# Kernel tuning notes

Hardware: AMD Instinct MI355X
Metric: run time of the kernel (lower is better)

## Reference

```python
import jax, jax.numpy as jnp
import numpy as np

B, L, D, H, K = 4, 2048, 256, 8, 32
DH = D // H
DE = 64          # d_edge
CLIP = 32        # relpos_clip


def _ln(x, g, b):
    mu = x.mean(-1, keepdims=True)
    var = ((x - mu) ** 2).mean(-1, keepdims=True)
    return (x - mu) / jnp.sqrt(var + 1e-5) * g + b


def _gelu(x):
    return jax.nn.gelu(x, approximate=False)  # torch nn.GELU default = exact erf


def _masked_softmax(logits, mask):
    logits = jnp.where(mask == 0, jnp.finfo(logits.dtype).min, logits)
    return jax.nn.softmax(logits, axis=-1)


def setup_inputs() -> dict:
    key = jax.random.key(0)
    ks = jax.random.split(key, 24)
    s = 0.02
    w = lambda i, shape: jax.random.normal(ks[i], shape, jnp.float32) * s
    p = {}
    p['x'] = jax.random.normal(ks[0], (B, L, D), jnp.float32)
    p['mask'] = jax.random.randint(ks[1], (B, L), 0, 2, jnp.int32)
    p['nbr_idx'] = jax.random.randint(ks[2], (B, L, K), 0, L, jnp.int32)
    p['nbr_mask'] = jax.random.randint(ks[3], (B, L, K), 0, 2, jnp.int32)
    p['rel_pos'] = jax.random.randint(ks[4], (B, L, K), 0, 2 * CLIP + 1, jnp.int32)
    p['g1'] = jnp.ones((D,)); p['b1'] = jnp.zeros((D,))
    p['wq'] = w(5, (D, D)); p['wk'] = w(6, (D, D)); p['wv'] = w(7, (D, D))
    p['relpos_emb'] = w(8, (2 * CLIP + 1, DE))
    p['we1'] = w(9, (DE, D)); p['be1'] = jnp.zeros((D,))
    p['we2'] = w(10, (D, 1)); p['be2'] = jnp.zeros((1,))
    p['wg1'] = w(11, (2 * D, D)); p['bg1'] = jnp.zeros((D,))
    p['wg2'] = w(12, (D, D)); p['bg2'] = jnp.zeros((D,))
    p['wlo'] = w(13, (D, D)); p['blo'] = jnp.zeros((D,))
    p['wqkv'] = w(14, (D, 3 * D)); p['wgo'] = w(15, (D, D))
    p['wf1'] = w(16, (D, D)); p['bf1'] = jnp.zeros((D,))
    p['wf2'] = w(17, (D, 2)); p['bf2'] = jnp.zeros((2,))
    p['g2'] = jnp.ones((D,)); p['b2'] = jnp.zeros((D,))
    p['wff1'] = w(18, (D, 4 * D)); p['bff1'] = jnp.zeros((4 * D,))
    p['wff2'] = w(19, (4 * D, D)); p['bff2'] = jnp.zeros((D,))
    return p


def _block(x, mask, nbr_idx, nbr_mask, rel_pos,
           g1, b1, wq, wk, wv, relpos_emb, we1, be1, we2, be2,
           wg1, bg1, wg2, bg2, wlo, blo, wqkv, wgo,
           wf1, bf1, wf2, bf2, g2, b2, wff1, bff1, wff2, bff2):
    mf = mask.astype(x.dtype)                       # [B,L]
    h = _ln(x, g1, b1)

    # ---- local graph attention (gather over K neighbors) ----
    neigh = jax.vmap(lambda hb, ib: hb[ib])(h, nbr_idx)     # [B,L,K,D]
    q = (h @ wq)[:, :, None, :]                             # [B,L,1,D]
    k = neigh @ wk                                          # [B,L,K,D]
    v = neigh @ wv
    attn = (q * k).sum(-1) / np.sqrt(D).astype(np.float32)  # [B,L,K]
    rel = jnp.clip(rel_pos, -CLIP, CLIP) + CLIP
    e = relpos_emb[rel]                                     # [B,L,K,DE]
    attn = attn + (_gelu(e @ we1 + be1) @ we2 + be2)[..., 0]
    amask = nbr_mask * mask[:, :, None]
    w = _masked_softmax(attn, amask)
    agg = jnp.einsum('blk,blkd->bld', w, v)
    agg = agg @ wlo + blo
    g = jax.nn.sigmoid(_gelu(jnp.concatenate([h, agg], -1) @ wg1 + bg1) @ wg2 + bg2)
    h_local = (h + g * agg) * mf[..., None]

    # ---- global linear attention ----
    qkv = h @ wqkv
    qg, kg, vg = jnp.split(qkv, 3, axis=-1)
    to_heads = lambda z: z.reshape(B, L, H, DH).transpose(0, 2, 1, 3)  # [B,H,L,DH]
    qg, kg, vg = to_heads(qg), to_heads(kg), to_heads(vg)
    phi = lambda z: jax.nn.elu(z) + 1.0
    qg, kg = phi(qg), phi(kg)
    m = mf[:, None, :, None]
    kg = kg * m
    vg = vg * m
    kv = jnp.einsum('bhld,bhlm->bhdm', kg, vg)
    z = 1.0 / (jnp.einsum('bhld,bhd->bhl', qg, kg.sum(axis=2)) + 1e-6)
    y = jnp.einsum('bhld,bhdm->bhlm', qg, kv) * z[..., None]
    y = y.transpose(0, 2, 1, 3).reshape(B, L, D)
    y = (y @ wgo) * mf[..., None]
    h_global = h + y

    # ---- gated fusion (softmax over 2 branches) ----
    fw = jax.nn.softmax(_gelu(h @ wf1 + bf1) @ wf2 + bf2, axis=-1)
    yc = fw[..., 0:1] * h_local + fw[..., 1:2] * h_global
    x2 = x + (yc - x)  # DropPath is identity in eval mode

    # ---- FFN ----
    hn = _ln(x2, g2, b2)
    ffn = _gelu(hn @ wff1 + bff1) @ wff2 + bff2
    out = (x2 + ffn) * mf[..., None]
    return out


def reference(x, mask, nbr_idx, nbr_mask, rel_pos,
              g1, b1, wq, wk, wv, relpos_emb, we1, be1, we2, be2,
              wg1, bg1, wg2, bg2, wlo, blo, wqkv, wgo,
              wf1, bf1, wf2, bf2, g2, b2, wff1, bff1, wff2, bff2):
    return _block(x, mask, nbr_idx, nbr_mask, rel_pos,
                  g1, b1, wq, wk, wv, relpos_emb, we1, be1, we2, be2,
                  wg1, bg1, wg2, bg2, wlo, blo, wqkv, wgo,
                  wf1, bf1, wf2, bf2, g2, b2, wff1, bff1, wff2, bff2)
```

## Files before the change

kernel.cpp:

```cpp
#include <hip/hip_runtime.h>
#include <math.h>

#define LSEQ 2048
#define BB 4
#define DD 256
#define NROWS (BB*LSEQ)
#define LDBIG 1792

typedef unsigned short u16;
typedef unsigned int u32;
typedef short s16x8 __attribute__((ext_vector_type(8)));
typedef float f32x4 __attribute__((ext_vector_type(4)));

#define WT_BIG  0
#define WT_LO   458752
#define WT_G1   524288
#define WT_G2   655360
#define WT_GO   720896
#define WT_FF1  786432
#define WT_FF2  1048576

__device__ __forceinline__ float gelu_f(float x){
    return 0.5f*x*(1.0f+erff(x*0.70710678118654752440f));
}
__device__ __forceinline__ float phi_f(float z){ return z>0.f ? z+1.f : expf(z); }
__device__ __forceinline__ float bf2f(u16 u){ union{u32 i; float f;} x; x.i = ((u32)u)<<16; return x.f; }
__device__ __forceinline__ u16 f2bf(float f){ union{float f; u32 i;} x; x.f = f; u32 r = (x.i + 0x7fff + ((x.i>>16)&1)) >> 16; return (u16)r; }

struct TransDesc { const float* src; int dstoff; int srcK; int N; int dstStride; int tstart; };
struct TransArgs { TransDesc d[11]; };

__global__ __launch_bounds__(256) void prep_kernel(
    TransArgs args, u16* __restrict__ WT,
    const float* __restrict__ x, const float* __restrict__ g1,
    const float* __restrict__ b1, u16* __restrict__ h,
    const float* __restrict__ emb, const float* __restrict__ we1,
    const float* __restrict__ be1, const float* __restrict__ we2,
    const float* __restrict__ be2, float* __restrict__ btab,
    float* __restrict__ kvz,
    const float* __restrict__ wlo, const float* __restrict__ wg1,
    const float* __restrict__ blo, const float* __restrict__ bg1,
    float* __restrict__ bprime)
{
    int bid = blockIdx.x;
    if (bid < 1216){
        int z = 0;
        #pragma unroll
        for (int i=1;i<11;++i) if (bid >= args.d[i].tstart) z = i;
        TransDesc e = args.d[z];
        int tid = bid - e.tstart;
        int ntx = e.N >> 5;
        int kt = tid / ntx, nt = tid - kt*ntx;
        __shared__ float tile[32][33];
        int tx = threadIdx.x & 31, ty = threadIdx.x >> 5;
        #pragma unroll
        for (int i=0;i<4;++i){
            int k = kt*32 + ty + i*8;
            tile[ty+i*8][tx] = e.src[(size_t)k*e.N + nt*32 + tx];
        }
        __syncthreads();
        #pragma unroll
        for (int i=0;i<4;++i){
            int n = nt*32 + ty + i*8;
            WT[e.dstoff + (size_t)n*e.dstStride + kt*32 + tx] = f2bf(tile[tx][ty+i*8]);
        }
    } else if (bid < 9408){
        int r = bid - 1216; int t = threadIdx.x;
        size_t i = (size_t)r*DD + t;
        float v = x[i];
        float s = v, ss = v*v;
        #pragma unroll
        for (int o=32;o>=1;o>>=1){ s += __shfl_xor(s,o); ss += __shfl_xor(ss,o); }
        __shared__ float sh[8];
        int wave = t>>6, lane = t&63;
        if (lane==0){ sh[wave]=s; sh[4+wave]=ss; }
        __syncthreads();
        float S  = sh[0]+sh[1]+sh[2]+sh[3];
        float SS = sh[4]+sh[5]+sh[6]+sh[7];
        float mu  = S*(1.f/DD);
        float var = SS*(1.f/DD) - mu*mu;
        float inv = rsqrtf(var + 1e-5f);
        h[i] = f2bf((v-mu)*inv*g1[t] + b1[t]);
    } else if (bid < 9473){
        int r = bid - 9408; int j = threadIdx.x;
        float acc = be1[j];
        #pragma unroll 8
        for (int d=0; d<64; ++d) acc += emb[r*64+d]*we1[d*256+j];
        float tv = gelu_f(acc)*we2[j];
        #pragma unroll
        for (int o=32;o>=1;o>>=1) tv += __shfl_xor(tv,o);
        __shared__ float sh2[4];
        int wave = j>>6, lane = j&63;
        if (lane==0) sh2[wave]=tv;
        __syncthreads();
        if (j==0) btab[r] = sh2[0]+sh2[1]+sh2[2]+sh2[3] + be2[0];
    } else if (bid < 9605){
        int idx = (bid - 9473)*256 + threadIdx.x;
        kvz[idx] = 0.f;
    } else if (bid < 9861){
        int n = bid - 9605; int t = threadIdx.x;
        __shared__ float shc[256];
        shc[t] = wg1[(size_t)(256+t)*256 + n];
        __syncthreads();
        const float* wr = wlo + (size_t)t*256;
        float a = 0.f;
        #pragma unroll 8
        for (int m=0;m<256;++m) a += wr[m]*shc[m];
        WT[WT_G1 + (size_t)n*512 + 256 + t] = f2bf(a);
    } else {
        int t = threadIdx.x;
        float a = bg1[t];
        for (int m=0;m<256;++m) a += blo[m]*wg1[(size_t)(256+m)*256 + t];
        bprime[t] = a;
    }
}

template<int ACT, bool FINAL, typename CT>
__device__ __forceinline__ void mgemm_core(
    const u16* __restrict__ A0, const u16* __restrict__ A1, int kswitch, int lda,
    const u16* __restrict__ WT, int Kd,
    const float* __restrict__ bias, int actcol,
    CT* __restrict__ C, int ldc,
    const u16* __restrict__ addsrc, const int* __restrict__ rowmask,
    int row0, int col0)
{
    __shared__ u16 ldsA[4096];
    __shared__ u16 ldsB[8192];
    int t = threadIdx.x;
    int l = t & 63, w = t >> 6;
    int wm = w >> 1, wn = w & 1;

    int s_ar = t >> 2, s_ao = t & 3;
    int aidx1 = (s_ar>>4)*1024 + s_ao*128 + (s_ar&15)*8;
    int aidx2 = aidx1 + 4*128;
    int s_bc = t >> 1, s_bo = (t & 1)*4;
    int bbase = (s_bc>>4)*1024 + (s_bc&15)*8;

    f32x4 acc[2][4];
    #pragma unroll
    for (int mf=0;mf<2;++mf)
        #pragma unroll
        for (int nf=0;nf<4;++nf)
            acc[mf][nf] = (f32x4){0.f,0.f,0.f,0.f};

    uint4 av1, av2, bv0, bv1, bv2, bv3;
    {
        const u16* ap = A0 + (size_t)(row0+s_ar)*lda;
        av1 = *(const uint4*)(ap + s_ao*8);
        av2 = *(const uint4*)(ap + 32 + s_ao*8);
        const u16* bp = WT + (size_t)(col0 + s_bc)*Kd + s_bo*8;
        bv0 = *(const uint4*)(bp); bv1 = *(const uint4*)(bp+8);
        bv2 = *(const uint4*)(bp+16); bv3 = *(const uint4*)(bp+24);
    }

    for (int k0 = 0; k0 < Kd; k0 += 64){
        __syncthreads();
        *(uint4*)&ldsA[aidx1] = av1;
        *(uint4*)&ldsA[aidx2] = av2;
        *(uint4*)&ldsB[bbase + (s_bo  )*128] = bv0;
        *(uint4*)&ldsB[bbase + (s_bo+1)*128] = bv1;
        *(uint4*)&ldsB[bbase + (s_bo+2)*128] = bv2;
        *(uint4*)&ldsB[bbase + (s_bo+3)*128] = bv3;
        __syncthreads();
        int kn = k0 + 64;
        if (kn < Kd){
            const u16* Ab = A0; int kk = kn;
            if (kn >= kswitch){ Ab = A1; kk = kn - kswitch; }
            const u16* ap = Ab + (size_t)(row0+s_ar)*lda + kk;
            av1 = *(const uint4*)(ap + s_ao*8);
            av2 = *(const uint4*)(ap + 32 + s_ao*8);
            const u16* bp = WT + (size_t)(col0 + s_bc)*Kd + kn + s_bo*8;
            bv0 = *(const uint4*)(bp); bv1 = *(const uint4*)(bp+8);
            bv2 = *(const uint4*)(bp+16); bv3 = *(const uint4*)(bp+24);
        }
        #pragma unroll
        for (int s=0;s<2;++s){
            s16x8 af[2], bfr[4];
            #pragma unroll
            for (int mf=0;mf<2;++mf) af[mf] = *(s16x8*)&ldsA[(wm*2+mf)*1024 + (s*4+(l>>4))*128 + (l&15)*8];
            #pragma unroll
            for (int nf=0;nf<4;++nf) bfr[nf] = *(s16x8*)&ldsB[(wn*4+nf)*1024 + (s*4+(l>>4))*128 + (l&15)*8];
            #pragma unroll
            for (int mf=0; mf<2; ++mf)
                #pragma unroll
                for (int nf=0; nf<4; ++nf)
                    acc[mf][nf] = __builtin_amdgcn_mfma_f32_16x16x32_bf16(af[mf], bfr[nf], acc[mf][nf], 0,0,0);
        }
    }

    int lrow = (l>>4)*4, lcol = l&15;
    #pragma unroll
    for (int mf=0; mf<2; ++mf){
        #pragma unroll
        for (int nf=0; nf<4; ++nf){
            int col = col0 + wn*64 + nf*16 + lcol;
            float bv;
            if (ACT==1) bv = (col >= actcol) ? bias[col-actcol] : 0.f;
            else        bv = bias ? bias[col] : 0.f;
            #pragma unroll
            for (int i=0;i<4;++i){
                int row = row0 + wm*32 + mf*16 + lrow + i;
                float v = acc[mf][nf][i] + bv;
                if (ACT==1){ if (col >= actcol) v = gelu_f(v); }
                else if (ACT==2) v = 1.f/(1.f+expf(-v));
                if (FINAL){
                    float mfv = (float)rowmask[row];
                    v = (bf2f(addsrc[(size_t)row*ldc + col]) + v) * mfv;
                }
                if constexpr (sizeof(CT)==2) C[(size_t)row*ldc+col] = (CT)f2bf(v);
                else                         C[(size_t)row*ldc+col] = v;
            }
        }
    }
}

template<int ACT, bool FINAL, typename CT>
__global__ __launch_bounds__(256) void mgemm(
    const u16* __restrict__ A0, const u16* __restrict__ A1, int kswitch, int lda,
    const u16* __restrict__ WT, int Kd,
    const float* __restrict__ bias, int actcol,
    CT* __restrict__ C, int ldc,
    const u16* __restrict__ addsrc, const int* __restrict__ rowmask)
{
    mgemm_core<ACT,FINAL,CT>(A0,A1,kswitch,lda,WT,Kd,bias,actcol,C,ldc,addsrc,rowmask,
                             blockIdx.x*64, blockIdx.y*128);
}

struct GemmCfg { const u16* A0; const u16* A1; int kswitch; const u16* WT; int Kd;
                 const float* bias; int act; u16* C; };
__global__ __launch_bounds__(256) void mgemm_tri(GemmCfg c0, GemmCfg c1, GemmCfg c2)
{
    GemmCfg c = (blockIdx.z==0) ? c0 : ((blockIdx.z==1) ? c1 : c2);
    if (c.act==1)
        mgemm_core<1,false,u16>(c.A0, c.A1, c.kswitch, 256, c.WT, c.Kd, c.bias, 0,
                                c.C, 256, nullptr, nullptr, blockIdx.x*64, blockIdx.y*128);
    else
        mgemm_core<0,false,u16>(c.A0, c.A1, c.kswitch, 256, c.WT, c.Kd, c.bias, 0,
                                c.C, 256, nullptr, nullptr, blockIdx.x*64, blockIdx.y*128);
}

__global__ __launch_bounds__(256) void lg_kernel(
    const u16* __restrict__ nb,
    const int* __restrict__ nbr_idx, const int* __restrict__ nbr_mask,
    const int* __restrict__ rel_pos, const int* __restrict__ mask,
    const float* __restrict__ btab, u16* __restrict__ agg,
    const float* __restrict__ kv, const float* __restrict__ ksum,
    u16* __restrict__ y)
{
    int bid = blockIdx.x;
    int xcd = bid & 7, pos = bid >> 3;
    int r = (xcd>>1)*2048 + (xcd&1)*1024 + pos;
    int b = r >> 11;
    int t = threadIdx.x, lane = t&63, wave = t>>6;
    __shared__ float s_w[32];
    __shared__ float s_agg[4][256];
    __shared__ float sq[256];
    uint2 qu = *(const uint2*)&nb[(size_t)r*LDBIG + lane*4];
    float q0 = bf2f(qu.x&0xffff), q1 = bf2f(qu.x>>16);
    float q2 = bf2f(qu.y&0xffff), q3 = bf2f(qu.y>>16);
    int mrow = mask[r];

    uint2 kreg[8], vreg[8];
    #pragma unroll
    for (int j=0;j<8;++j){
        int idx = nbr_idx[r*32 + wave*8 + j];
        size_t grow = ((size_t)(b<<11) + idx)*LDBIG;
        kreg[j] = *(const uint2*)&nb[grow + 256 + lane*4];
        vreg[j] = *(const uint2*)&nb[grow + 512 + lane*4];
    }
    float d[8];
    #pragma unroll
    for (int j=0;j<8;++j){
        d[j] = q0*bf2f(kreg[j].x&0xffff) + q1*bf2f(kreg[j].x>>16)
             + q2*bf2f(kreg[j].y&0xffff) + q3*bf2f(kreg[j].y>>16);
    }
    #define CMB(a,b,s) ({ float _t = (lane&(s)) ? (a) : (b); float _r = __shfl_xor(_t,(s)); (lane&(s)) ? ((b)+_r) : ((a)+_r); })
    float e10 = CMB(d[0],d[1],1), e11 = CMB(d[2],d[3],1);
    float e12 = CMB(d[4],d[5],1), e13 = CMB(d[6],d[7],1);
    float e20 = CMB(e10,e11,2),   e21 = CMB(e12,e13,2);
    float e3  = CMB(e20,e21,4);
    #undef CMB
    e3 += __shfl_xor(e3,8); e3 += __shfl_xor(e3,16); e3 += __shfl_xor(e3,32);
    if (lane < 8){
        int k = wave*8 + lane;
        int rp = rel_pos[r*32+k];
        rp = rp < -32 ? -32 : (rp > 32 ? 32 : rp);
        float logit = e3*0.0625f + btab[rp+32];
        int am = nbr_mask[r*32+k] * mrow;
        s_w[k] = am ? logit : -3.402823466e38f;
    }
    if (t < 128){
        u32 u = *(const u32*)&nb[(size_t)r*LDBIG + 768 + t*2];
        sq[t*2]   = phi_f(bf2f((u16)(u & 0xffff)));
        sq[t*2+1] = phi_f(bf2f((u16)(u >> 16)));
    }
    __syncthreads();
    if (wave==0){
        float lg = (lane<32) ? s_w[lane] : -3.402823466e38f;
        float m = lg;
        #pragma unroll
        for (int o=16;o>=1;o>>=1) m = fmaxf(m, __shfl_xor(m,o));
        float e = (lane<32) ? expf(lg-m) : 0.f;
        float ssum = e;
        #pragma unroll
        for (int o=16;o>=1;o>>=1) ssum += __shfl_xor(ssum,o);
        if (lane<32) s_w[lane] = e/ssum;
    }
    __syncthreads();
    float4 av = {0.f,0.f,0.f,0.f};
    #pragma unroll
    for (int j=0;j<8;++j){
        float wk = s_w[wave*8 + j];
        av.x += wk*bf2f(vreg[j].x&0xffff); av.y += wk*bf2f(vreg[j].x>>16);
        av.z += wk*bf2f(vreg[j].y&0xffff); av.w += wk*bf2f(vreg[j].y>>16);
    }
    *(float4*)&s_agg[wave][lane*4] = av;
    __syncthreads();
    float sum = s_agg[0][t]+s_agg[1][t]+s_agg[2][t]+s_agg[3][t];
    agg[(size_t)r*256 + t] = f2bf(sum);

    int hh = t>>5, m = t&31;
    const float* kvb = &kv[(size_t)((b<<3)+hh)*1024 + m];
    const float* ksb = &ksum[((b<<3)+hh)*32];
    const float* sqh = &sq[hh*32];
    float acc=0.f, az=0.f;
    #pragma unroll
    for (int dd=0; dd<32; ++dd){
        float qd = sqh[dd];
        acc += qd * kvb[dd*32];
        az  += qd * ksb[dd];
    }
    y[(size_t)r*256 + t] = f2bf(acc / (az + 1e-6f));
}

__global__ __launch_bounds__(256) void linstats_kernel(
    const u16* __restrict__ qkv, const int* __restrict__ mask,
    float* __restrict__ kv, float* __restrict__ ksum)
{
    int blk = blockIdx.x;
    int bh = blk >> 6, ch = blk & 63;
    int b = bh >> 3, hh = bh & 7;
    int t = threadIdx.x;
    int d = t >> 3, m4 = (t & 7)*4;
    __shared__ float sk[8][32], sv[8][32];
    float a0=0,a1=0,a2=0,a3=0, aks=0;
    int l0 = ch*32;
    int half = t >> 7, tt = t & 127;
    int lr = tt >> 4, e2 = (tt & 15)*2;
    for (int g8=0; g8<4; ++g8){
        int l = l0 + g8*8 + lr;
        size_t base = ((size_t)b*LSEQ + l)*LDBIG + (half ? 1280 : 1024) + hh*32 + e2;
        u32 u = *(const u32*)&qkv[base];
        float mf = (float)mask[b*LSEQ + l];
        float x0 = bf2f((u16)(u & 0xffff));
        float x1 = bf2f((u16)(u >> 16));
        if (half==0){ sk[lr][e2] = phi_f(x0)*mf; sk[lr][e2+1] = phi_f(x1)*mf; }
        else        { sv[lr][e2] = x0*mf;        sv[lr][e2+1] = x1*mf; }
        __syncthreads();
        #pragma unroll
        for (int rr=0;rr<8;++rr){
            float kd = sk[rr][d];
            a0 += kd*sv[rr][m4]; a1 += kd*sv[rr][m4+1];
            a2 += kd*sv[rr][m4+2]; a3 += kd*sv[rr][m4+3];
            if ((t&7)==0) aks += kd;
        }
        __syncthreads();
    }
    size_t kb = (size_t)bh*1024 + d*32 + m4;
    atomicAdd(&kv[kb+0],a0); atomicAdd(&kv[kb+1],a1);
    atomicAdd(&kv[kb+2],a2); atomicAdd(&kv[kb+3],a3);
    if ((t&7)==0) atomicAdd(&ksum[bh*32+d], aks);
}

__global__ __launch_bounds__(128) void combine_kernel(
    const u16* __restrict__ h, const u16* __restrict__ agglo,
    const u16* __restrict__ g, const u16* __restrict__ ygo,
    const u16* __restrict__ bigout, const float* __restrict__ wf2,
    const float* __restrict__ bf2v, const int* __restrict__ mask,
    const float* __restrict__ g2, const float* __restrict__ b2,
    u16* __restrict__ x2, u16* __restrict__ hn)
{
    int r = blockIdx.x, t = threadIdx.x;
    int wave = t>>6, lane = t&63;
    u32 fu = *(const u32*)&bigout[(size_t)r*LDBIG + 1536 + t*2];
    float fa = bf2f((u16)(fu&0xffff)), fb = bf2f((u16)(fu>>16));
    int dd = t*2;
    float p0 = fa*wf2[dd*2]   + fb*wf2[dd*2+2];
    float p1 = fa*wf2[dd*2+1] + fb*wf2[dd*2+3];
    #pragma unroll
    for (int o=32;o>=1;o>>=1){ p0 += __shfl_xor(p0,o); p1 += __shfl_xor(p1,o); }
    __shared__ float shp[4];
    if (lane==0){ shp[wave]=p0; shp[2+wave]=p1; }
    __syncthreads();
    float P0 = shp[0]+shp[1]+bf2v[0], P1 = shp[2]+shp[3]+bf2v[1];
    float mx = fmaxf(P0,P1);
    float e0 = expf(P0-mx), e1 = expf(P1-mx);
    float f0 = e0/(e0+e1), f1v = e1/(e0+e1);
    size_t i = (size_t)r*DD + t*2;
    float mf = (float)mask[r];
    u32 hu = *(const u32*)&h[i],  au = *(const u32*)&agglo[i];
    u32 gu = *(const u32*)&g[i],  yu = *(const u32*)&ygo[i];
    float hv0 = bf2f((u16)(hu&0xffff)), hv1 = bf2f((u16)(hu>>16));
    float ag0 = bf2f((u16)(au&0xffff)), ag1 = bf2f((u16)(au>>16));
    float gg0 = bf2f((u16)(gu&0xffff)), gg1 = bf2f((u16)(gu>>16));
    float yy0 = bf2f((u16)(yu&0xffff)), yy1 = bf2f((u16)(yu>>16));
    float v0 = f0*((hv0 + gg0*ag0)*mf) + f1v*(hv0 + yy0*mf);
    float v1 = f0*((hv1 + gg1*ag1)*mf) + f1v*(hv1 + yy1*mf);
    *(u32*)&x2[i] = (u32)f2bf(v0) | ((u32)f2bf(v1)<<16);
    float s = v0+v1, ss = v0*v0+v1*v1;
    #pragma unroll
    for (int o=32;o>=1;o>>=1){ s += __shfl_xor(s,o); ss += __shfl_xor(ss,o); }
    __shared__ float sh[4];
    if (lane==0){ sh[wave]=s; sh[2+wave]=ss; }
    __syncthreads();
    float S  = sh[0]+sh[1];
    float SS = sh[2]+sh[3];
    float mu  = S*(1.f/DD);
    float var = SS*(1.f/DD) - mu*mu;
    float inv = rsqrtf(var + 1e-5f);
    int j0 = t*2;
    float o0 = (v0-mu)*inv*g2[j0]   + b2[j0];
    float o1 = (v1-mu)*inv*g2[j0+1] + b2[j0+1];
    *(u32*)&hn[i] = (u32)f2bf(o0) | ((u32)f2bf(o1)<<16);
}

extern "C" void kernel_launch(void* const* d_in, const int* in_sizes, int n_in,
                              void* d_out, int out_size, void* d_ws, size_t ws_size,
                              hipStream_t stream)
{
    const float* x        = (const float*)d_in[0];
    const int*   mask     = (const int*)  d_in[1];
    const int*   nbr_idx  = (const int*)  d_in[2];
    const int*   nbr_mask = (const int*)  d_in[3];
    const int*   rel_pos  = (const int*)  d_in[4];
    const float* g1   = (const float*)d_in[5];
    const float* b1   = (const float*)d_in[6];
    const float* wq   = (const float*)d_in[7];
    const float* wk   = (const float*)d_in[8];
    const float* wv   = (const float*)d_in[9];
    const float* relpos_emb = (const float*)d_in[10];
    const float* we1  = (const float*)d_in[11];
    const float* be1  = (const float*)d_in[12];
    const float* we2  = (const float*)d_in[13];
    const float* be2  = (const float*)d_in[14];
    const float* wg1  = (const float*)d_in[15];
    const float* bg1  = (const float*)d_in[16];
    const float* wg2  = (const float*)d_in[17];
    const float* bg2  = (const float*)d_in[18];
    const float* wlo  = (const float*)d_in[19];
    const float* blo  = (const float*)d_in[20];
    const float* wqkv = (const float*)d_in[21];
    const float* wgo  = (const float*)d_in[22];
    const float* wf1  = (const float*)d_in[23];
    const float* bf1  = (const float*)d_in[24];
    const float* wf2  = (const float*)d_in[25];
    const float* bf2  = (const float*)d_in[26];
    const float* g2   = (const float*)d_in[27];
    const float* b2   = (const float*)d_in[28];
    const float* wff1 = (const float*)d_in[29];
    const float* bff1 = (const float*)d_in[30];
    const float* wff2 = (const float*)d_in[31];
    const float* bff2 = (const float*)d_in[32];
    float* out = (float*)d_out;

    unsigned char* wsb = (unsigned char*)d_ws;
    u16* bigout  = (u16*)(wsb + ((size_t)0<<20));
    u16* h_bf    = (u16*)(wsb + ((size_t)30<<20));
    u16* agg_bf  = (u16*)(wsb + ((size_t)34<<20));
    u16* agglo_bf= (u16*)(wsb + ((size_t)38<<20));
    u16* x2y_bf  = (u16*)(wsb + ((size_t)42<<20));
    u16* tg_bf   = (u16*)(wsb + ((size_t)46<<20));
    u16* ygo_bf  = (u16*)(wsb + ((size_t)50<<20));
    u16* hn_bf   = (u16*)(wsb + ((size_t)54<<20));
    u16* WT      = (u16*)(wsb + ((size_t)58<<20));
    float* btab  = (float*)(wsb + ((size_t)61<<20));
    float* kvb   = btab + 128;
    float* ksb   = kvb + 32768;
    float* bprime= ksb + 1024;

    TransArgs ta;
    ta.d[0]  = { wq,   WT_BIG + 0,        256,  256,  256,    0 };
    ta.d[1]  = { wk,   WT_BIG + 65536,    256,  256,  256,   64 };
    ta.d[2]  = { wv,   WT_BIG + 131072,   256,  256,  256,  128 };
    ta.d[3]  = { wqkv, WT_BIG + 196608,   256,  768,  256,  192 };
    ta.d[4]  = { wf1,  WT_BIG + 393216,   256,  256,  256,  384 };
    ta.d[5]  = { wlo,  WT_LO,             256,  256,  256,  448 };
    ta.d[6]  = { wg1,  WT_G1,             256,  256,  512,  512 };
    ta.d[7]  = { wg2,  WT_G2,             256,  256,  256,  576 };
    ta.d[8]  = { wgo,  WT_GO,             256,  256,  256,  640 };
    ta.d[9]  = { wff1, WT_FF1,            256, 1024,  256,  704 };
    ta.d[10] = { wff2, WT_FF2,           1024,  256, 1024,  960 };

    const int KBIG = 1<<30;
    dim3 blk(256);

    prep_kernel<<<9862, blk, 0, stream>>>(ta, WT, x, g1, b1, h_bf,
                                          relpos_emb, we1, be1, we2, be2, btab, kvb,
                                          wlo, wg1, blo, bg1, bprime);
    mgemm<1,false,u16><<<dim3(128,14), blk, 0, stream>>>(h_bf, h_bf, KBIG, 256, WT+WT_BIG, 256, bf1, 1536, bigout, LDBIG, nullptr, nullptr);
    linstats_kernel<<<2048, blk, 0, stream>>>(bigout, mask, kvb, ksb);
    lg_kernel<<<NROWS, blk, 0, stream>>>(bigout, nbr_idx, nbr_mask, rel_pos, mask, btab,
                                         agg_bf, kvb, ksb, x2y_bf);
    {
        GemmCfg cgo = { x2y_bf, x2y_bf, KBIG, WT+WT_GO, 256, nullptr, 0, ygo_bf };
        GemmCfg clo = { agg_bf, agg_bf, KBIG, WT+WT_LO, 256, blo,     0, agglo_bf };
        GemmCfg cg1 = { h_bf,   agg_bf, 256,  WT+WT_G1, 512, bprime,  1, tg_bf };
        mgemm_tri<<<dim3(128,2,3), blk, 0, stream>>>(cgo, clo, cg1);
    }
    mgemm<2,false,u16><<<dim3(128,2), blk, 0, stream>>>(tg_bf, tg_bf, KBIG, 256, WT+WT_G2, 256, bg2, 0, agg_bf, 256, nullptr, nullptr);
    combine_kernel<<<NROWS, dim3(128), 0, stream>>>(h_bf, agglo_bf, agg_bf, ygo_bf, bigout, wf2, bf2, mask, g2, b2, x2y_bf, hn_bf);
    mgemm<1,false,u16><<<dim3(128,8), blk, 0, stream>>>(hn_bf, hn_bf, KBIG, 256, WT+WT_FF1, 256, bff1, 0, bigout, 1024, nullptr, nullptr);
    mgemm<0,true,float><<<dim3(128,2), blk, 0, stream>>>(bigout, bigout, KBIG, 1024, WT+WT_FF2, 1024, bff2, 0, out, 256, x2y_bf, mask);
}
```

Measured before the change: 317.1 us.

## Compute wlo·wg1 product via MFMA GEMM and split linear-attention apply out of gather kernel

```diff
diff --git a/kernel.cpp b/kernel.cpp
--- a/kernel.cpp
+++ b/kernel.cpp
@@ -19,6 +19,8 @@
 #define WT_GO   720896
 #define WT_FF1  786432
 #define WT_FF2  1048576
+#define WT_TMP1 1310720
+#define WT_TMP2 1376256
 
 __device__ __forceinline__ float gelu_f(float x){
     return 0.5f*x*(1.0f+erff(x*0.70710678118654752440f));
@@ -28,7 +30,7 @@
 __device__ __forceinline__ u16 f2bf(float f){ union{float f; u32 i;} x; x.f = f; u32 r = (x.i + 0x7fff + ((x.i>>16)&1)) >> 16; return (u16)r; }
 
 struct TransDesc { const float* src; int dstoff; int srcK; int N; int dstStride; int tstart; };
-struct TransArgs { TransDesc d[11]; };
+struct TransArgs { TransDesc d[12]; };
 
 __global__ __launch_bounds__(256) void prep_kernel(
     TransArgs args, u16* __restrict__ WT,
@@ -43,10 +45,10 @@
     float* __restrict__ bprime)
 {
     int bid = blockIdx.x;
-    if (bid < 1216){
+    if (bid < 1280){
         int z = 0;
         #pragma unroll
-        for (int i=1;i<11;++i) if (bid >= args.d[i].tstart) z = i;
+        for (int i=1;i<12;++i) if (bid >= args.d[i].tstart) z = i;
         TransDesc e = args.d[z];
         int tid = bid - e.tstart;
         int ntx = e.N >> 5;
@@ -64,8 +66,8 @@
             int n = nt*32 + ty + i*8;
             WT[e.dstoff + (size_t)n*e.dstStride + kt*32 + tx] = f2bf(tile[tx][ty+i*8]);
         }
-    } else if (bid < 9408){
-        int r = bid - 1216; int t = threadIdx.x;
+    } else if (bid < 9472){
+        int r = bid - 1280; int t = threadIdx.x;
         size_t i = (size_t)r*DD + t;
         float v = x[i];
         float s = v, ss = v*v;
@@ -81,8 +83,8 @@
         float var = SS*(1.f/DD) - mu*mu;
         float inv = rsqrtf(var + 1e-5f);
         h[i] = f2bf((v-mu)*inv*g1[t] + b1[t]);
-    } else if (bid < 9473){
-        int r = bid - 9408; int j = threadIdx.x;
+    } else if (bid < 9537){
+        int r = bid - 9472; int j = threadIdx.x;
         float acc = be1[j];
         #pragma unroll 8
         for (int d=0; d<64; ++d) acc += emb[r*64+d]*we1[d*256+j];
@@ -94,19 +96,16 @@
         if (lane==0) sh2[wave]=tv;
         __syncthreads();
         if (j==0) btab[r] = sh2[0]+sh2[1]+sh2[2]+sh2[3] + be2[0];
-    } else if (bid < 9605){
-        int idx = (bid - 9473)*256 + threadIdx.x;
+    } else if (bid < 9669){
+        int idx = (bid - 9537)*256 + threadIdx.x;
         kvz[idx] = 0.f;
-    } else if (bid < 9861){
-        int n = bid - 9605; int t = threadIdx.x;
-        __shared__ float shc[256];
-        shc[t] = wg1[(size_t)(256+t)*256 + n];
-        __syncthreads();
-        const float* wr = wlo + (size_t)t*256;
-        float a = 0.f;
-        #pragma unroll 8
-        for (int m=0;m<256;++m) a += wr[m]*shc[m];
-        WT[WT_G1 + (size_t)n*512 + 256 + t] = f2bf(a);
+    } else if (bid < 9733){
+        int idx = (bid - 9669)*1024 + threadIdx.x*4;
+        float4 v = *(const float4*)&wlo[idx];
+        u32 lo = (u32)f2bf(v.x) | ((u32)f2bf(v.y)<<16);
+        u32 hi = (u32)f2bf(v.z) | ((u32)f2bf(v.w)<<16);
+        *(u32*)&WT[WT_TMP2 + idx]     = lo;
+        *(u32*)&WT[WT_TMP2 + idx + 2] = hi;
     } else {
         int t = threadIdx.x;
         float a = bg1[t];
@@ -239,22 +238,17 @@
                                 c.C, 256, nullptr, nullptr, blockIdx.x*64, blockIdx.y*128);
 }
 
-__global__ __launch_bounds__(256) void lg_kernel(
+__global__ __launch_bounds__(256) void nattn_kernel(
     const u16* __restrict__ nb,
     const int* __restrict__ nbr_idx, const int* __restrict__ nbr_mask,
     const int* __restrict__ rel_pos, const int* __restrict__ mask,
-    const float* __restrict__ btab, u16* __restrict__ agg,
-    const float* __restrict__ kv, const float* __restrict__ ksum,
-    u16* __restrict__ y)
-{
-    int bid = blockIdx.x;
-    int xcd = bid & 7, pos = bid >> 3;
-    int r = (xcd>>1)*2048 + (xcd&1)*1024 + pos;
+    const float* __restrict__ btab, u16* __restrict__ agg)
+{
+    int r = blockIdx.x;
     int b = r >> 11;
     int t = threadIdx.x, lane = t&63, wave = t>>6;
     __shared__ float s_w[32];
     __shared__ float s_agg[4][256];
-    __shared__ float sq[256];
     uint2 qu = *(const uint2*)&nb[(size_t)r*LDBIG + lane*4];
     float q0 = bf2f(qu.x&0xffff), q1 = bf2f(qu.x>>16);
     float q2 = bf2f(qu.y&0xffff), q3 = bf2f(qu.y>>16);
@@ -289,11 +283,6 @@
         int am = nbr_mask[r*32+k] * mrow;
         s_w[k] = am ? logit : -3.402823466e38f;
     }
-    if (t < 128){
-        u32 u = *(const u32*)&nb[(size_t)r*LDBIG + 768 + t*2];
-        sq[t*2]   = phi_f(bf2f((u16)(u & 0xffff)));
-        sq[t*2+1] = phi_f(bf2f((u16)(u >> 16)));
-    }
     __syncthreads();
     if (wave==0){
         float lg = (lane<32) ? s_w[lane] : -3.402823466e38f;
@@ -318,19 +307,6 @@
     __syncthreads();
     float sum = s_agg[0][t]+s_agg[1][t]+s_agg[2][t]+s_agg[3][t];
     agg[(size_t)r*256 + t] = f2bf(sum);
-
-    int hh = t>>5, m = t&31;
-    const float* kvb = &kv[(size_t)((b<<3)+hh)*1024 + m];
-    const float* ksb = &ksum[((b<<3)+hh)*32];
-    const float* sqh = &sq[hh*32];
-    float acc=0.f, az=0.f;
-    #pragma unroll
-    for (int dd=0; dd<32; ++dd){
-        float qd = sqh[dd];
-        acc += qd * kvb[dd*32];
-        az  += qd * ksb[dd];
-    }
-    y[(size_t)r*256 + t] = f2bf(acc / (az + 1e-6f));
 }
 
 __global__ __launch_bounds__(256) void linstats_kernel(
@@ -338,16 +314,16 @@
     float* __restrict__ kv, float* __restrict__ ksum)
 {
     int blk = blockIdx.x;
-    int bh = blk >> 6, ch = blk & 63;
+    int bh = blk >> 4, ch = blk & 15;
     int b = bh >> 3, hh = bh & 7;
     int t = threadIdx.x;
     int d = t >> 3, m4 = (t & 7)*4;
     __shared__ float sk[8][32], sv[8][32];
     float a0=0,a1=0,a2=0,a3=0, aks=0;
-    int l0 = ch*32;
+    int l0 = ch*128;
     int half = t >> 7, tt = t & 127;
     int lr = tt >> 4, e2 = (tt & 15)*2;
-    for (int g8=0; g8<4; ++g8){
+    for (int g8=0; g8<16; ++g8){
         int l = l0 + g8*8 + lr;
         size_t base = ((size_t)b*LSEQ + l)*LDBIG + (half ? 1280 : 1024) + hh*32 + e2;
         u32 u = *(const u32*)&qkv[base];
@@ -370,6 +346,33 @@
     atomicAdd(&kv[kb+0],a0); atomicAdd(&kv[kb+1],a1);
     atomicAdd(&kv[kb+2],a2); atomicAdd(&kv[kb+3],a3);
     if ((t&7)==0) atomicAdd(&ksum[bh*32+d], aks);
+}
+
+__global__ __launch_bounds__(256) void linapply_kernel(
+    const u16* __restrict__ qkv, const float* __restrict__ kv,
+    const float* __restrict__ ksum, u16* __restrict__ y)
+{
+    int r = blockIdx.x; int b = r >> 11;
+    int t = threadIdx.x;
+    __shared__ float sq[256];
+    if (t < 128){
+        u32 u = *(const u32*)&qkv[(size_t)r*LDBIG + 768 + t*2];
+        sq[t*2]   = phi_f(bf2f((u16)(u & 0xffff)));
+        sq[t*2+1] = phi_f(bf2f((u16)(u >> 16)));
+    }
+    __syncthreads();
+    int hh = t>>5, m = t&31;
+    const float* kvb = &kv[(size_t)((b<<3)+hh)*1024 + m];
+    const float* ksb = &ksum[((b<<3)+hh)*32];
+    const float* sqh = &sq[hh*32];
+    float acc=0.f, az=0.f;
+    #pragma unroll
+    for (int dd=0; dd<32; ++dd){
+        float qd = sqh[dd];
+        acc += qd * kvb[dd*32];
+        az  += qd * ksb[dd];
+    }
+    y[(size_t)r*256 + t] = f2bf(acc / (az + 1e-6f));
 }
 
 __global__ __launch_bounds__(128) void combine_kernel(
@@ -479,28 +482,32 @@
     float* bprime= ksb + 1024;
 
     TransArgs ta;
-    ta.d[0]  = { wq,   WT_BIG + 0,        256,  256,  256,    0 };
-    ta.d[1]  = { wk,   WT_BIG + 65536,    256,  256,  256,   64 };
-    ta.d[2]  = { wv,   WT_BIG + 131072,   256,  256,  256,  128 };
-    ta.d[3]  = { wqkv, WT_BIG + 196608,   256,  768,  256,  192 };
-    ta.d[4]  = { wf1,  WT_BIG + 393216,   256,  256,  256,  384 };
-    ta.d[5]  = { wlo,  WT_LO,             256,  256,  256,  448 };
-    ta.d[6]  = { wg1,  WT_G1,             256,  256,  512,  512 };
-    ta.d[7]  = { wg2,  WT_G2,             256,  256,  256,  576 };
-    ta.d[8]  = { wgo,  WT_GO,             256,  256,  256,  640 };
-    ta.d[9]  = { wff1, WT_FF1,            256, 1024,  256,  704 };
-    ta.d[10] = { wff2, WT_FF2,           1024,  256, 1024,  960 };
+    ta.d[0]  = { wq,          WT_BIG + 0,       256,  256,  256,    0 };
+    ta.d[1]  = { wk,          WT_BIG + 65536,   256,  256,  256,   64 };
+    ta.d[2]  = { wv,          WT_BIG + 131072,  256,  256,  256,  128 };
+    ta.d[3]  = { wqkv,        WT_BIG + 196608,  256,  768,  256,  192 };
+    ta.d[4]  = { wf1,         WT_BIG + 393216,  256,  256,  256,  384 };
+    ta.d[5]  = { wlo,         WT_LO,            256,  256,  256,  448 };
+    ta.d[6]  = { wg1,         WT_G1,            256,  256,  512,  512 };
+    ta.d[7]  = { wg2,         WT_G2,            256,  256,  256,  576 };
+    ta.d[8]  = { wgo,         WT_GO,            256,  256,  256,  640 };
+    ta.d[9]  = { wff1,        WT_FF1,           256, 1024,  256,  704 };
+    ta.d[10] = { wff2,        WT_FF2,          1024,  256, 1024,  960 };
+    ta.d[11] = { wg1+65536,   WT_TMP1,          256,  256,  256, 1216 };
 
     const int KBIG = 1<<30;
     dim3 blk(256);
 
-    prep_kernel<<<9862, blk, 0, stream>>>(ta, WT, x, g1, b1, h_bf,
+    prep_kernel<<<9734, blk, 0, stream>>>(ta, WT, x, g1, b1, h_bf,
                                           relpos_emb, we1, be1, we2, be2, btab, kvb,
                                           wlo, wg1, blo, bg1, bprime);
+    mgemm<0,false,u16><<<dim3(4,2), blk, 0, stream>>>(WT+WT_TMP1, WT+WT_TMP1, KBIG, 256,
+                                                      WT+WT_TMP2, 256, nullptr, 0,
+                                                      WT+WT_G1+256, 512, nullptr, nullptr);
     mgemm<1,false,u16><<<dim3(128,14), blk, 0, stream>>>(h_bf, h_bf, KBIG, 256, WT+WT_BIG, 256, bf1, 1536, bigout, LDBIG, nullptr, nullptr);
-    linstats_kernel<<<2048, blk, 0, stream>>>(bigout, mask, kvb, ksb);
-    lg_kernel<<<NROWS, blk, 0, stream>>>(bigout, nbr_idx, nbr_mask, rel_pos, mask, btab,
-                                         agg_bf, kvb, ksb, x2y_bf);
+    linstats_kernel<<<512, blk, 0, stream>>>(bigout, mask, kvb, ksb);
+    linapply_kernel<<<NROWS, blk, 0, stream>>>(bigout, kvb, ksb, x2y_bf);
+    nattn_kernel<<<NROWS, blk, 0, stream>>>(bigout, nbr_idx, nbr_mask, rel_pos, mask, btab, agg_bf);
     {
         GemmCfg cgo = { x2y_bf, x2y_bf, KBIG, WT+WT_GO, 256, nullptr, 0, ygo_bf };
         GemmCfg clo = { agg_bf, agg_bf, KBIG, WT+WT_LO, 256, blo,     0, agglo_bf };
```

New measurement: 285.2 us. -10.1%, faster.
